# Kernel optimization log

Hardware: AMD Instinct MI355X
Metric: run time of the kernel (lower is better)

Reference implementation:

```python
import jax, jax.numpy as jnp
import numpy as np

N = 100000        # nodes
E = 1600000       # edges (avg degree 16)
H = 128           # gnn_hidden_size
F_NODE = 4        # node_features (forced to 4 by _validate_and_fix_data)
F_EDGE = 2        # edge_features (forced to 2)
L = 3             # gnn_layers
BN_EPS = 1e-5
NORM_EPS = 1e-12


def _sage_layer(h, src, dst, eattr, Wn, Ws, gamma, beta):
    # message: lin_neighbor(concat(x_j, edge_attr)) where x_j = h[src]
    msg = jnp.concatenate([h[src], eattr], axis=-1) @ Wn          # [E+N, H]
    agg = jax.ops.segment_sum(msg, dst, num_segments=N)           # scatter-sum
    cnt = jax.ops.segment_sum(jnp.ones(dst.shape[0], h.dtype), dst, num_segments=N)
    agg = agg / jnp.maximum(cnt, 1.0)[:, None]                    # mean aggregation
    out = jax.nn.relu(agg + h @ Ws)                               # self-loop linear + ReLU
    # BatchNorm1d (batch statistics, biased var)
    mean = out.mean(axis=0)
    var = out.var(axis=0)
    out = (out - mean) * jax.lax.rsqrt(var + BN_EPS) * gamma + beta
    # dropout = identity (eval); L2 normalize per node
    nrm = jnp.maximum(jnp.linalg.norm(out, axis=-1, keepdims=True), NORM_EPS)
    return out / nrm


def setup_inputs() -> dict:
    key = jax.random.key(0)
    ks = jax.random.split(key, 24)
    s = 0.05
    inp = {
        "x": jax.random.normal(ks[0], (N, F_NODE), jnp.float32),
        "edge_index": jax.random.randint(ks[1], (2, E), 0, N, dtype=jnp.int32),
        "edge_attr": jax.random.uniform(ks[2], (E, F_EDGE), jnp.float32),
        "W_in": jax.random.normal(ks[3], (F_NODE, H), jnp.float32) * s,
        "b_in": jnp.zeros((H,), jnp.float32),
        "W_jump": jax.random.normal(ks[4], (L * H, H), jnp.float32) * s,
        "b_jump": jnp.zeros((H,), jnp.float32),
        "W1": jax.random.normal(ks[5], (H, H // 2), jnp.float32) * s,
        "b1": jnp.zeros((H // 2,), jnp.float32),
        "W2": jax.random.normal(ks[6], (H // 2, 1), jnp.float32) * s,
        "b2": jnp.zeros((1,), jnp.float32),
    }
    for l in range(L):
        inp[f"Wn_{l}"] = jax.random.normal(ks[7 + 4 * l], (H + F_EDGE, H), jnp.float32) * s
        inp[f"Ws_{l}"] = jax.random.normal(ks[8 + 4 * l], (H, H), jnp.float32) * s
        inp[f"gamma_{l}"] = jnp.ones((H,), jnp.float32)
        inp[f"beta_{l}"] = jnp.zeros((H,), jnp.float32)
    return inp


def reference(x, edge_index, edge_attr, W_in, b_in,
              Wn_0, Ws_0, gamma_0, beta_0,
              Wn_1, Ws_1, gamma_1, beta_1,
              Wn_2, Ws_2, gamma_2, beta_2,
              W_jump, b_jump, W1, b1, W2, b2):
    # add self loops (with zero edge_attr), as in _safe_add_self_loops
    loop = jnp.arange(N, dtype=edge_index.dtype)
    src = jnp.concatenate([edge_index[0], loop])
    dst = jnp.concatenate([edge_index[1], loop])
    eattr = jnp.concatenate([edge_attr, jnp.zeros((N, F_EDGE), edge_attr.dtype)], axis=0)

    h = x @ W_in + b_in                                          # input_projection
    layer_params = [(Wn_0, Ws_0, gamma_0, beta_0),
                    (Wn_1, Ws_1, gamma_1, beta_1),
                    (Wn_2, Ws_2, gamma_2, beta_2)]
    layer_outputs = []
    for Wn, Ws, gamma, beta in layer_params:
        h = _sage_layer(h, src, dst, eattr, Wn, Ws, gamma, beta)
        layer_outputs.append(h)
    # jump (skip) connection: concat all layer outputs -> Linear -> ReLU
    h = jax.nn.relu(jnp.concatenate(layer_outputs, axis=-1) @ W_jump + b_jump)
    # neighbor_scorer: Linear -> ReLU -> Linear -> scalar per node
    scores = jax.nn.relu(h @ W1 + b1) @ W2 + b2                  # [N, 1]
    return scores[:, 0]
```

## Files before the change

### kernel.cpp

```cpp
#include <hip/hip_runtime.h>


#define HDIM 128

using f16x8 = __attribute__((ext_vector_type(8))) _Float16;
using f32x4 = __attribute__((ext_vector_type(4))) float;

__device__ inline unsigned pack_f16x2(float a, float b) {
  _Float16 ha = (_Float16)a, hb = (_Float16)b;
  unsigned short ua = __builtin_bit_cast(unsigned short, ha);
  unsigned short ub = __builtin_bit_cast(unsigned short, hb);
  return (unsigned)ua | ((unsigned)ub << 16);
}
__device__ inline float2 unpack_f16x2(unsigned u) {
  _Float16 lo = __builtin_bit_cast(_Float16, (unsigned short)(u & 0xffffu));
  _Float16 hi = __builtin_bit_cast(_Float16, (unsigned short)(u >> 16));
  return make_float2((float)lo, (float)hi);
}

__global__ __launch_bounds__(256) void count_kernel(
    const int* __restrict__ dst, int* __restrict__ cnt,
    int* __restrict__ rank, int E) {
  int e = blockIdx.x * 256 + threadIdx.x;
  if (e >= E) return;
  rank[e] = atomicAdd(&cnt[dst[e]], 1);
}

__global__ __launch_bounds__(128) void scan_block_sum(
    const int* __restrict__ cnt, int* __restrict__ bsum, int N) {
  __shared__ int sd[128];
  int t = threadIdx.x;
  int i = blockIdx.x * 128 + t;
  sd[t] = (i < N) ? cnt[i] : 0;
  __syncthreads();
  for (int off = 64; off > 0; off >>= 1) {
    if (t < off) sd[t] += sd[t + off];
    __syncthreads();
  }
  if (t == 0) bsum[blockIdx.x] = sd[0];
}

__global__ __launch_bounds__(256) void scan_partials(
    const int* __restrict__ bsum, int* __restrict__ boff, int nch) {
  __shared__ int sd[256];
  int t = threadIdx.x;
  int base = t * 4;
  int v0 = (base + 0 < nch) ? bsum[base + 0] : 0;
  int v1 = (base + 1 < nch) ? bsum[base + 1] : 0;
  int v2 = (base + 2 < nch) ? bsum[base + 2] : 0;
  int v3 = (base + 3 < nch) ? bsum[base + 3] : 0;
  sd[t] = v0 + v1 + v2 + v3;
  __syncthreads();
  for (int off = 1; off < 256; off <<= 1) {
    int x = sd[t];
    int y = (t >= off) ? sd[t - off] : 0;
    __syncthreads();
    sd[t] = x + y;
    __syncthreads();
  }
  int run = (t == 0) ? 0 : sd[t - 1];
  if (base + 0 < nch) boff[base + 0] = run; run += v0;
  if (base + 1 < nch) boff[base + 1] = run; run += v1;
  if (base + 2 < nch) boff[base + 2] = run; run += v2;
  if (base + 3 < nch) boff[base + 3] = run;
}

__global__ __launch_bounds__(128) void scan_final(
    const int* __restrict__ cnt, const int* __restrict__ boff,
    int* __restrict__ rs, int N) {
  __shared__ int sd[128];
  int t = threadIdx.x, b = blockIdx.x;
  int i = b * 128 + t;
  int v = (i < N) ? cnt[i] : 0;
  sd[t] = v;
  __syncthreads();
  for (int off = 1; off < 128; off <<= 1) {
    int x = sd[t];
    int y = (t >= off) ? sd[t - off] : 0;
    __syncthreads();
    sd[t] = x + y;
    __syncthreads();
  }
  if (i < N) rs[i] = boff[b] + ((t == 0) ? 0 : sd[t - 1]);
}

__global__ __launch_bounds__(256) void fill_kernel(
    const int* __restrict__ src, const int* __restrict__ dst,
    const float* __restrict__ ea, const int* __restrict__ rs,
    const int* __restrict__ rank, uint2* __restrict__ cidx2, int E) {
  int e = blockIdx.x * 256 + threadIdx.x;
  if (e >= E) return;
  int d = dst[e];
  float2 v = *reinterpret_cast<const float2*>(&ea[2 * (size_t)e]);
  int pos = rs[d] + rank[e];
  cidx2[pos] = make_uint2((unsigned)src[e], pack_f16x2(v.x, v.y));
}

__global__ __launch_bounds__(256) void aggx_kernel(
    const float* __restrict__ x, const int* __restrict__ rs,
    const int* __restrict__ cnt, const uint2* __restrict__ cidx2,
    float* __restrict__ aggx, float* __restrict__ eagg, int N) {
  int i = blockIdx.x * 256 + threadIdx.x;
  if (i >= N) return;
  float4 a = *reinterpret_cast<const float4*>(&x[(size_t)i * 4]);
  float4 b = make_float4(0.f, 0.f, 0.f, 0.f);
  float e0 = 0.f, e1 = 0.f, f0 = 0.f, f1 = 0.f;
  int p = rs[i], e = p + cnt[i];
  for (; p + 1 < e; p += 2) {
    uint2 c0 = cidx2[p], c1 = cidx2[p + 1];
    float4 v0 = *reinterpret_cast<const float4*>(&x[(size_t)c0.x * 4]);
    float4 v1 = *reinterpret_cast<const float4*>(&x[(size_t)c1.x * 4]);
    float2 u0 = unpack_f16x2(c0.y);
    float2 u1 = unpack_f16x2(c1.y);
    a.x += v0.x; a.y += v0.y; a.z += v0.z; a.w += v0.w;
    b.x += v1.x; b.y += v1.y; b.z += v1.z; b.w += v1.w;
    e0 += u0.x; e1 += u0.y;
    f0 += u1.x; f1 += u1.y;
  }
  if (p < e) {
    uint2 c0 = cidx2[p];
    float4 v0 = *reinterpret_cast<const float4*>(&x[(size_t)c0.x * 4]);
    float2 u0 = unpack_f16x2(c0.y);
    a.x += v0.x; a.y += v0.y; a.z += v0.z; a.w += v0.w;
    e0 += u0.x; e1 += u0.y;
  }
  a.x += b.x; a.y += b.y; a.z += b.z; a.w += b.w;
  *reinterpret_cast<float4*>(&aggx[(size_t)i * 4]) = a;
  eagg[2 * (size_t)i + 0] = e0 + f0;
  eagg[2 * (size_t)i + 1] = e1 + f1;
}

__global__ __launch_bounds__(256) void pack_weights_kernel(
    const float* __restrict__ Wn0, const float* __restrict__ Ws0,
    const float* __restrict__ Wn1, const float* __restrict__ Ws1,
    const float* __restrict__ Wn2, const float* __restrict__ Ws2,
    const float* __restrict__ Wj, _Float16* __restrict__ outp) {
  int i = blockIdx.x * 256 + threadIdx.x;
  if (i >= 147456) return;
  int j = i & 7, lane = (i >> 3) & 63;
  float v;
  if (i < 98304) {
    int l = i >> 15;
    int r = i & 32767;
    int nt = (r >> 9) & 7, kt = r >> 12;
    int k = kt * 32 + (lane >> 4) * 8 + j;
    int n = nt * 16 + (lane & 15);
    const float* Wn = (l == 0) ? Wn0 : (l == 1) ? Wn1 : Wn2;
    const float* Ws = (l == 0) ? Ws0 : (l == 1) ? Ws1 : Ws2;
    v = (k < 128) ? Wn[(size_t)k * HDIM + n] : Ws[(size_t)(k - 128) * HDIM + n];
  } else {
    int r = i - 98304;
    int nt = (r >> 9) & 7, kt = r >> 12;
    int k = kt * 32 + (lane >> 4) * 8 + j;
    int n = nt * 16 + (lane & 15);
    v = Wj[(size_t)k * HDIM + n];
  }
  outp[i] = (_Float16)v;
}

template <bool L0>
__global__ __launch_bounds__(256) void sage_mfma_kernel(
    const float* __restrict__ A0f, const float* __restrict__ A1f,
    const _Float16* __restrict__ Hprev, const int* __restrict__ rs,
    const uint2* __restrict__ cidx2,
    const float* __restrict__ Wi, const float* __restrict__ bi,
    const float* __restrict__ eagg, const int* __restrict__ cnt,
    const _Float16* __restrict__ Bp, const float* __restrict__ Wn,
    _Float16* __restrict__ outh, float* __restrict__ bnstat, int N) {
  __shared__ _Float16 sA[64 * 256];
  __shared__ float sE[128];
  __shared__ float sBNs[4][128];
  __shared__ float sBNq[4][128];
  const int t = threadIdx.x;
  const int base = blockIdx.x * 64;

  if (t < 64) {
    int grow = base + t;
    float e0 = 0.f, e1 = 0.f;
    if (grow < N) {
      float inv = 1.0f / ((float)cnt[grow] + 1.0f);
      e0 = eagg[2 * (size_t)grow] * inv;
      e1 = eagg[2 * (size_t)grow + 1] * inv;
    }
    sE[2 * t] = e0;
    sE[2 * t + 1] = e1;
  }

  if (L0) {
#pragma unroll
    for (int it = 0; it < 8; ++it) {
      int c = t + it * 256;
      int row = c >> 5, k8 = c & 31;
      int grow = base + row;
      f16x8 hv = {};
      if (grow < N) {
        float inv = 1.0f / ((float)cnt[grow] + 1.0f);
        float scale = (k8 < 16) ? inv : 1.0f;
        const float* rp = (k8 < 16) ? &A0f[(size_t)grow * 4] : &A1f[(size_t)grow * 4];
        float4 r = *reinterpret_cast<const float4*>(rp);
        int col0 = (k8 & 15) * 8;
#pragma unroll
        for (int jj = 0; jj < 8; ++jj) {
          int col = col0 + jj;
          hv[jj] = (_Float16)(bi[col] + scale * (r.x * Wi[col] + r.y * Wi[HDIM + col] +
                                                 r.z * Wi[2 * HDIM + col] + r.w * Wi[3 * HDIM + col]));
        }
      }
      int byte = (row * 512 + k8 * 16) ^ ((row & 7) << 4);
      *reinterpret_cast<f16x8*>(reinterpret_cast<char*>(sA) + byte) = hv;
    }
  } else {
    const int row = t >> 2, o = t & 3;
    const int grow = base + row;
    float acc[32];
#pragma unroll
    for (int c = 0; c < 32; ++c) acc[c] = 0.f;
    f16x8 selfv[4] = {};
    if (grow < N) {
      const char* selfrow = reinterpret_cast<const char*>(Hprev + (size_t)grow * HDIM);
#pragma unroll
      for (int j = 0; j < 4; ++j) {
        selfv[j] = *reinterpret_cast<const f16x8*>(selfrow + j * 64 + o * 16);
#pragma unroll
        for (int jj = 0; jj < 8; ++jj) acc[j * 8 + jj] = (float)selfv[j][jj];
      }
      int p = rs[grow];
      const int cn = cnt[grow];
      int e = p + cn;
      for (; p + 3 < e; p += 4) {
        uint2 q0 = cidx2[p], q1 = cidx2[p + 1], q2 = cidx2[p + 2], q3 = cidx2[p + 3];
        const char* m0 = reinterpret_cast<const char*>(Hprev + (size_t)q0.x * HDIM) + o * 16;
        const char* m1 = reinterpret_cast<const char*>(Hprev + (size_t)q1.x * HDIM) + o * 16;
        const char* m2 = reinterpret_cast<const char*>(Hprev + (size_t)q2.x * HDIM) + o * 16;
        const char* m3 = reinterpret_cast<const char*>(Hprev + (size_t)q3.x * HDIM) + o * 16;
        f16x8 c0[4], c1[4], c2[4], c3[4];
#pragma unroll
        for (int j = 0; j < 4; ++j) c0[j] = *reinterpret_cast<const f16x8*>(m0 + j * 64);
#pragma unroll
        for (int j = 0; j < 4; ++j) c1[j] = *reinterpret_cast<const f16x8*>(m1 + j * 64);
#pragma unroll
        for (int j = 0; j < 4; ++j) c2[j] = *reinterpret_cast<const f16x8*>(m2 + j * 64);
#pragma unroll
        for (int j = 0; j < 4; ++j) c3[j] = *reinterpret_cast<const f16x8*>(m3 + j * 64);
#pragma unroll
        for (int j = 0; j < 4; ++j)
#pragma unroll
          for (int jj = 0; jj < 8; ++jj)
            acc[j * 8 + jj] += ((float)c0[j][jj] + (float)c1[j][jj]) +
                               ((float)c2[j][jj] + (float)c3[j][jj]);
      }
      for (; p < e; ++p) {
        uint2 q0 = cidx2[p];
        const char* m0 = reinterpret_cast<const char*>(Hprev + (size_t)q0.x * HDIM) + o * 16;
#pragma unroll
        for (int j = 0; j < 4; ++j) {
          f16x8 c0 = *reinterpret_cast<const f16x8*>(m0 + j * 64);
#pragma unroll
          for (int jj = 0; jj < 8; ++jj) acc[j * 8 + jj] += (float)c0[jj];
        }
      }
      float inv = 1.0f / ((float)cn + 1.0f);
#pragma unroll
      for (int c = 0; c < 32; ++c) acc[c] *= inv;
    }
    const int swz = (row & 7) << 4;
#pragma unroll
    for (int j = 0; j < 4; ++j) {
      f16x8 av;
#pragma unroll
      for (int jj = 0; jj < 8; ++jj) av[jj] = (_Float16)acc[j * 8 + jj];
      int k8a = o + j * 4;
      *reinterpret_cast<f16x8*>(reinterpret_cast<char*>(sA) +
                                ((row * 512 + k8a * 16) ^ swz)) = av;
      int k8h = 16 + o + j * 4;
      *reinterpret_cast<f16x8*>(reinterpret_cast<char*>(sA) +
                                ((row * 512 + k8h * 16) ^ swz)) = selfv[j];
    }
  }
  __syncthreads();

  const int lane = t & 63;
  const int w = t >> 6;
  const int col16 = lane & 15;
  const int kgrp = lane >> 4;
  f32x4 acc[8];
#pragma unroll
  for (int nt = 0; nt < 8; ++nt) acc[nt] = (f32x4){0.f, 0.f, 0.f, 0.f};

  const int arow = w * 16 + col16;
  const int aswz = (arow & 7) << 4;
#pragma unroll
  for (int kt = 0; kt < 8; ++kt) {
    int abyte = (arow * 512 + kt * 64 + kgrp * 16) ^ aswz;
    f16x8 a = *reinterpret_cast<const f16x8*>(reinterpret_cast<const char*>(sA) + abyte);
    const f16x8* bp = reinterpret_cast<const f16x8*>(Bp) + (size_t)kt * 512 + lane;
#pragma unroll
    for (int nt = 0; nt < 8; ++nt) {
      f16x8 b = bp[nt * 64];
      acc[nt] = __builtin_amdgcn_mfma_f32_16x16x32_f16(a, b, acc[nt], 0, 0, 0);
    }
  }

#pragma unroll
  for (int nt = 0; nt < 8; ++nt) {
    int col = nt * 16 + col16;
    float we0 = Wn[(size_t)128 * HDIM + col];
    float we1 = Wn[(size_t)129 * HDIM + col];
    float s = 0.f, q = 0.f;
#pragma unroll
    for (int i = 0; i < 4; ++i) {
      int lr = w * 16 + kgrp * 4 + i;
      int row = base + lr;
      if (row < N) {
        float v = acc[nt][i] + sE[2 * lr] * we0 + sE[2 * lr + 1] * we1;
        v = fmaxf(v, 0.f);
        outh[(size_t)row * HDIM + col] = (_Float16)v;
        s += v;
        q += v * v;
      }
    }
    s += __shfl_xor(s, 16, 64);
    s += __shfl_xor(s, 32, 64);
    q += __shfl_xor(q, 16, 64);
    q += __shfl_xor(q, 32, 64);
    if (lane < 16) {
      sBNs[w][col] = s;
      sBNq[w][col] = q;
    }
  }
  __syncthreads();
  if (t < 128) {
    float s = sBNs[0][t] + sBNs[1][t] + sBNs[2][t] + sBNs[3][t];
    float q = sBNq[0][t] + sBNq[1][t] + sBNq[2][t] + sBNq[3][t];
    atomicAdd(&bnstat[t], s);
    atomicAdd(&bnstat[HDIM + t], q);
  }
}

__global__ __launch_bounds__(256) void bn_l2_kernel(
    const _Float16* __restrict__ outh, const float* __restrict__ stat,
    const float* __restrict__ gamma, const float* __restrict__ beta,
    float invN, _Float16* __restrict__ h, int N) {
  __shared__ float sAB[256];
  int t = threadIdx.x;
  if (t < 128) {
    float mean = stat[t] * invN;
    float var = stat[128 + t] * invN - mean * mean;
    float A = gamma[t] / sqrtf(var + 1e-5f);
    sAB[t] = A;
    sAB[128 + t] = beta[t] - mean * A;
  }
  __syncthreads();
  int i = blockIdx.x * 4 + (t >> 6);
  if (i >= N) return;
  int lane = t & 63;
  unsigned u = (reinterpret_cast<const unsigned*>(outh + (size_t)i * HDIM))[lane];
  float2 v = unpack_f16x2(u);
  float A0 = sAB[lane * 2 + 0], A1 = sAB[lane * 2 + 1];
  float B0 = sAB[128 + lane * 2 + 0], B1 = sAB[128 + lane * 2 + 1];
  float y0 = v.x * A0 + B0;
  float y1 = v.y * A1 + B1;
  float s = y0 * y0 + y1 * y1;
#pragma unroll
  for (int m = 32; m > 0; m >>= 1) s += __shfl_xor(s, m, 64);
  float inv = 1.0f / fmaxf(sqrtf(s), 1e-12f);
  (reinterpret_cast<unsigned*>(h + (size_t)i * HDIM))[lane] =
      pack_f16x2(y0 * inv, y1 * inv);
}

__global__ __launch_bounds__(256) void jump_mfma_kernel(
    const _Float16* __restrict__ h1, const _Float16* __restrict__ h2,
    const _Float16* __restrict__ h3, const _Float16* __restrict__ Bp,
    const float* __restrict__ bj, const float* __restrict__ W1p,
    const float* __restrict__ b1p, const float* __restrict__ W2p,
    const float* __restrict__ b2p, float* __restrict__ outp, int N) {
  __shared__ _Float16 sA[64 * 384];
  const int t = threadIdx.x;
  const int base = blockIdx.x * 64;

  const _Float16* hs[3] = {h1, h2, h3};
#pragma unroll
  for (int it = 0; it < 12; ++it) {
    int c = t + it * 256;
    int row = c / 48, k8 = c % 48;
    int grow = base + row;
    f16x8 hv = {};
    if (grow < N)
      hv = (reinterpret_cast<const f16x8*>(hs[k8 >> 4] + (size_t)grow * HDIM))[k8 & 15];
    int byte = (row * 768 + k8 * 16) ^ ((row & 7) << 4);
    *reinterpret_cast<f16x8*>(reinterpret_cast<char*>(sA) + byte) = hv;
  }
  __syncthreads();

  const int lane = t & 63;
  const int w = t >> 6;
  const int col16 = lane & 15;
  const int kgrp = lane >> 4;
  f32x4 acc[8];
#pragma unroll
  for (int nt = 0; nt < 8; ++nt) acc[nt] = (f32x4){0.f, 0.f, 0.f, 0.f};

  const int arow = w * 16 + col16;
  const int aswz = (arow & 7) << 4;
#pragma unroll
  for (int kt = 0; kt < 12; ++kt) {
    int abyte = (arow * 768 + kt * 64 + kgrp * 16) ^ aswz;
    f16x8 a = *reinterpret_cast<const f16x8*>(reinterpret_cast<const char*>(sA) + abyte);
    const f16x8* bp = reinterpret_cast<const f16x8*>(Bp) + (size_t)kt * 512 + lane;
#pragma unroll
    for (int nt = 0; nt < 8; ++nt) {
      f16x8 b = bp[nt * 64];
      acc[nt] = __builtin_amdgcn_mfma_f32_16x16x32_f16(a, b, acc[nt], 0, 0, 0);
    }
  }
  __syncthreads();

  float* sG = reinterpret_cast<float*>(sA);
  float* sS = sG + 64 * 128;
#pragma unroll
  for (int nt = 0; nt < 8; ++nt) {
    int col = nt * 16 + col16;
    float bb = bj[col];
#pragma unroll
    for (int i = 0; i < 4; ++i) {
      int lr = w * 16 + kgrp * 4 + i;
      sG[lr * 128 + col] = fmaxf(acc[nt][i] + bb, 0.f);
    }
  }
  __syncthreads();

  const int m = t & 63, grp = t >> 6;
  float a2[16];
#pragma unroll
  for (int i = 0; i < 16; ++i) a2[i] = b1p[m];
#pragma unroll 4
  for (int k = 0; k < 128; ++k) {
    float wv = W1p[(size_t)k * 64 + m];
#pragma unroll
    for (int i = 0; i < 16; ++i) a2[i] += sG[(grp * 16 + i) * 128 + k] * wv;
  }
#pragma unroll
  for (int i = 0; i < 16; ++i) sS[(grp * 16 + i) * 64 + m] = fmaxf(a2[i], 0.f);
  __syncthreads();

  if (t < 64) {
    int row = base + t;
    if (row < N) {
      float s = b2p[0];
#pragma unroll 8
      for (int mm = 0; mm < 64; ++mm) s += sS[t * 64 + mm] * W2p[mm];
      outp[row] = s;
    }
  }
}

extern "C" void kernel_launch(void* const* d_in, const int* in_sizes, int n_in,
                              void* d_out, int out_size, void* d_ws, size_t ws_size,
                              hipStream_t stream) {
  const float* x      = (const float*)d_in[0];
  const int*   ei     = (const int*)d_in[1];
  const float* eattr  = (const float*)d_in[2];
  const float* W_in   = (const float*)d_in[3];
  const float* b_in   = (const float*)d_in[4];
  const float* W_jump = (const float*)d_in[5];
  const float* b_jump = (const float*)d_in[6];
  const float* W1     = (const float*)d_in[7];
  const float* b1     = (const float*)d_in[8];
  const float* W2     = (const float*)d_in[9];
  const float* b2     = (const float*)d_in[10];
  const float* Wn[3] = {(const float*)d_in[11], (const float*)d_in[15], (const float*)d_in[19]};
  const float* Ws[3] = {(const float*)d_in[12], (const float*)d_in[16], (const float*)d_in[20]};
  const float* gm[3] = {(const float*)d_in[13], (const float*)d_in[17], (const float*)d_in[21]};
  const float* bt[3] = {(const float*)d_in[14], (const float*)d_in[18], (const float*)d_in[22]};

  const int N = in_sizes[0] / 4;
  const int E = in_sizes[2] / 2;
  const int* srcp = ei;
  const int* dstp = ei + (size_t)E;
  const int nch = (N + 127) / 128;
  const size_t nh = (size_t)N * HDIM;

  char* wsb = (char*)d_ws;
  size_t off = 0;
  auto carve = [&](size_t bytes) -> void* {
    void* p = wsb + off;
    off = (off + bytes + 255) & ~(size_t)255;
    return p;
  };
  _Float16* h1   = (_Float16*)carve(nh * 2);
  _Float16* h2   = (_Float16*)carve(nh * 2);
  _Float16* h3   = (_Float16*)carve(nh * 2);
  _Float16* outh = (_Float16*)carve(nh * 2);
  float*    aggx = (float*)carve((size_t)N * 4 * 4);
  float*    eagg = (float*)carve((size_t)N * 2 * 4);
  int*      cnt  = (int*)carve((size_t)N * 4);
  int*      rowstart = (int*)carve((size_t)N * 4);
  int*      rank     = (int*)carve((size_t)E * 4);
  uint2*    cidx2    = (uint2*)carve((size_t)E * 8);
  int*      bsum = (int*)carve(4096);
  int*      boff = (int*)carve(4096);
  float*    bnstat = (float*)carve(3 * 256 * sizeof(float));
  _Float16* wpack  = (_Float16*)carve(147456 * 2);

  hipMemsetAsync(cnt, 0, (size_t)N * sizeof(int), stream);
  hipMemsetAsync(bnstat, 0, 3 * 256 * sizeof(float), stream);
  count_kernel<<<(E + 255) / 256, 256, 0, stream>>>(dstp, cnt, rank, E);
  pack_weights_kernel<<<(147456 + 255) / 256, 256, 0, stream>>>(
      Wn[0], Ws[0], Wn[1], Ws[1], Wn[2], Ws[2], W_jump, wpack);
  scan_block_sum<<<nch, 128, 0, stream>>>(cnt, bsum, N);
  scan_partials<<<1, 256, 0, stream>>>(bsum, boff, nch);
  scan_final<<<nch, 128, 0, stream>>>(cnt, boff, rowstart, N);
  fill_kernel<<<(E + 255) / 256, 256, 0, stream>>>(srcp, dstp, eattr, rowstart, rank, cidx2, E);

  const int gemm_grid = (N + 63) / 64;
  const float invN = 1.0f / (float)N;

  aggx_kernel<<<(N + 255) / 256, 256, 0, stream>>>(x, rowstart, cnt, cidx2, aggx, eagg, N);
  sage_mfma_kernel<true><<<gemm_grid, 256, 0, stream>>>(
      aggx, x, nullptr, rowstart, cidx2, W_in, b_in, eagg, cnt, wpack, Wn[0],
      outh, bnstat, N);
  bn_l2_kernel<<<(N + 3) / 4, 256, 0, stream>>>(outh, bnstat, gm[0], bt[0], invN, h1, N);

  _Float16* hbuf[3] = {h1, h2, h3};
  for (int l = 1; l < 3; ++l) {
    sage_mfma_kernel<false><<<gemm_grid, 256, 0, stream>>>(
        nullptr, nullptr, hbuf[l - 1], rowstart, cidx2, nullptr, nullptr, eagg, cnt,
        wpack + (size_t)l * 32768, Wn[l], outh, bnstat + 256 * l, N);
    bn_l2_kernel<<<(N + 3) / 4, 256, 0, stream>>>(outh, bnstat + 256 * l,
                                                  gm[l], bt[l], invN, hbuf[l], N);
  }

  jump_mfma_kernel<<<gemm_grid, 256, 0, stream>>>(h1, h2, h3, wpack + 98304, b_jump,
                                                  W1, b1, W2, b2, (float*)d_out, N);
}
```

Before: 556.6 us.

## Shard degree-count atomics and process nodes in degree-sorted order

Count atomics are spread over 8 shard copies of the count array to cut contention, then summed, with per-shard offsets used in the CSR fill. A degree histogram and counting sort build a permutation so the aggregation kernels handle nodes of similar degree together, reducing wavefront divergence in the gather loops. The fill uses nontemporal stores. The trade-off is several extra small kernels, an 8x larger count buffer, and scattered output rows in the sage kernel.

```diff
diff --git a/kernel.cpp b/kernel.cpp
--- a/kernel.cpp
+++ b/kernel.cpp
@@ -2,6 +2,7 @@
 
 
 #define HDIM 128
+#define DEGB 512
 
 using f16x8 = __attribute__((ext_vector_type(8))) _Float16;
 using f32x4 = __attribute__((ext_vector_type(4))) float;
@@ -19,11 +20,32 @@
 }
 
 __global__ __launch_bounds__(256) void count_kernel(
-    const int* __restrict__ dst, int* __restrict__ cnt,
-    int* __restrict__ rank, int E) {
+    const int* __restrict__ dst, int* __restrict__ cnt8,
+    int* __restrict__ rank, int E, int N) {
   int e = blockIdx.x * 256 + threadIdx.x;
   if (e >= E) return;
-  rank[e] = atomicAdd(&cnt[dst[e]], 1);
+  int shard = blockIdx.x & 7;
+  rank[e] = atomicAdd(&cnt8[(size_t)shard * N + dst[e]], 1);
+}
+
+__global__ __launch_bounds__(256) void sum8_kernel(
+    int* __restrict__ cnt8, int* __restrict__ cnt, int N) {
+  int i = blockIdx.x * 256 + threadIdx.x;
+  if (i >= N) return;
+  int v[8];
+  int s = 0;
+#pragma unroll
+  for (int k = 0; k < 8; ++k) {
+    v[k] = cnt8[(size_t)k * N + i];
+    s += v[k];
+  }
+  cnt[i] = s;
+  int run = 0;
+#pragma unroll
+  for (int k = 0; k < 8; ++k) {
+    cnt8[(size_t)k * N + i] = run;
+    run += v[k];
+  }
 }
 
 __global__ __launch_bounds__(128) void scan_block_sum(
@@ -84,24 +106,79 @@
   if (i < N) rs[i] = boff[b] + ((t == 0) ? 0 : sd[t - 1]);
 }
 
+__global__ __launch_bounds__(256) void deg_hist_kernel(
+    const int* __restrict__ cnt, int* __restrict__ hist, int N) {
+  __shared__ int lh[DEGB];
+  int t = threadIdx.x;
+  for (int k = t; k < DEGB; k += 256) lh[k] = 0;
+  __syncthreads();
+  int i = blockIdx.x * 256 + t;
+  if (i < N) {
+    int d = cnt[i];
+    if (d > DEGB - 1) d = DEGB - 1;
+    atomicAdd(&lh[d], 1);
+  }
+  __syncthreads();
+  for (int k = t; k < DEGB; k += 256)
+    if (lh[k]) atomicAdd(&hist[k], lh[k]);
+}
+
+__global__ __launch_bounds__(256) void deg_scan_kernel(
+    const int* __restrict__ hist, int* __restrict__ degcur) {
+  __shared__ int sd[DEGB];
+  int t = threadIdx.x;
+  sd[t] = hist[t];
+  sd[t + 256] = hist[t + 256];
+  __syncthreads();
+  if (t == 0) {
+    int run = 0;
+    for (int k = 0; k < DEGB; ++k) {
+      int v = sd[k];
+      sd[k] = run;
+      run += v;
+    }
+  }
+  __syncthreads();
+  degcur[t] = sd[t];
+  degcur[t + 256] = sd[t + 256];
+}
+
+__global__ __launch_bounds__(256) void deg_scatter_kernel(
+    const int* __restrict__ cnt, int* __restrict__ degcur,
+    int* __restrict__ perm, int N) {
+  int i = blockIdx.x * 256 + threadIdx.x;
+  if (i >= N) return;
+  int d = cnt[i];
+  if (d > DEGB - 1) d = DEGB - 1;
+  int pos = atomicAdd(&degcur[d], 1);
+  perm[pos] = i;
+}
+
 __global__ __launch_bounds__(256) void fill_kernel(
     const int* __restrict__ src, const int* __restrict__ dst,
     const float* __restrict__ ea, const int* __restrict__ rs,
-    const int* __restrict__ rank, uint2* __restrict__ cidx2, int E) {
+    const int* __restrict__ cnt8, const int* __restrict__ rank,
+    unsigned long long* __restrict__ cidx2, int E, int N) {
   int e = blockIdx.x * 256 + threadIdx.x;
   if (e >= E) return;
+  int shard = blockIdx.x & 7;
   int d = dst[e];
   float2 v = *reinterpret_cast<const float2*>(&ea[2 * (size_t)e]);
-  int pos = rs[d] + rank[e];
-  cidx2[pos] = make_uint2((unsigned)src[e], pack_f16x2(v.x, v.y));
+  int pos = rs[d] + cnt8[(size_t)shard * N + d] + rank[e];
+  unsigned long long u =
+      (unsigned long long)(unsigned)src[e] |
+      ((unsigned long long)pack_f16x2(v.x, v.y) << 32);
+  __builtin_nontemporal_store(u, cidx2 + pos);
 }
 
 __global__ __launch_bounds__(256) void aggx_kernel(
     const float* __restrict__ x, const int* __restrict__ rs,
     const int* __restrict__ cnt, const uint2* __restrict__ cidx2,
+    const int* __restrict__ perm,
     float* __restrict__ aggx, float* __restrict__ eagg, int N) {
-  int i = blockIdx.x * 256 + threadIdx.x;
-  if (i >= N) return;
+  int idx = blockIdx.x * 256 + threadIdx.x;
+  if (idx >= N) return;
+  int i = perm[idx];
   float4 a = *reinterpret_cast<const float4*>(&x[(size_t)i * 4]);
   float4 b = make_float4(0.f, 0.f, 0.f, 0.f);
   float e0 = 0.f, e1 = 0.f, f0 = 0.f, f1 = 0.f;
@@ -162,7 +239,7 @@
 __global__ __launch_bounds__(256) void sage_mfma_kernel(
     const float* __restrict__ A0f, const float* __restrict__ A1f,
     const _Float16* __restrict__ Hprev, const int* __restrict__ rs,
-    const uint2* __restrict__ cidx2,
+    const uint2* __restrict__ cidx2, const int* __restrict__ perm,
     const float* __restrict__ Wi, const float* __restrict__ bi,
     const float* __restrict__ eagg, const int* __restrict__ cnt,
     const _Float16* __restrict__ Bp, const float* __restrict__ Wn,
@@ -175,9 +252,10 @@
   const int base = blockIdx.x * 64;
 
   if (t < 64) {
-    int grow = base + t;
+    int gidx = base + t;
     float e0 = 0.f, e1 = 0.f;
-    if (grow < N) {
+    if (gidx < N) {
+      int grow = L0 ? gidx : perm[gidx];
       float inv = 1.0f / ((float)cnt[grow] + 1.0f);
       e0 = eagg[2 * (size_t)grow] * inv;
       e1 = eagg[2 * (size_t)grow + 1] * inv;
@@ -211,12 +289,13 @@
     }
   } else {
     const int row = t >> 2, o = t & 3;
-    const int grow = base + row;
+    const int gidx = base + row;
     float acc[32];
 #pragma unroll
     for (int c = 0; c < 32; ++c) acc[c] = 0.f;
     f16x8 selfv[4] = {};
-    if (grow < N) {
+    if (gidx < N) {
+      const int grow = perm[gidx];
       const char* selfrow = reinterpret_cast<const char*>(Hprev + (size_t)grow * HDIM);
 #pragma unroll
       for (int j = 0; j < 4; ++j) {
@@ -310,8 +389,9 @@
 #pragma unroll
     for (int i = 0; i < 4; ++i) {
       int lr = w * 16 + kgrp * 4 + i;
-      int row = base + lr;
-      if (row < N) {
+      int gidx = base + lr;
+      if (gidx < N) {
+        int row = L0 ? gidx : perm[gidx];
         float v = acc[nt][i] + sE[2 * lr] * we0 + sE[2 * lr + 1] * we1;
         v = fmaxf(v, 0.f);
         outh[(size_t)row * HDIM + col] = (_Float16)v;
@@ -494,38 +574,50 @@
   float*    aggx = (float*)carve((size_t)N * 4 * 4);
   float*    eagg = (float*)carve((size_t)N * 2 * 4);
   int*      cnt  = (int*)carve((size_t)N * 4);
+  int*      cnt8 = (int*)carve((size_t)N * 8 * 4);
   int*      rowstart = (int*)carve((size_t)N * 4);
+  int*      perm     = (int*)carve((size_t)N * 4);
   int*      rank     = (int*)carve((size_t)E * 4);
-  uint2*    cidx2    = (uint2*)carve((size_t)E * 8);
+  unsigned long long* cidx2 = (unsigned long long*)carve((size_t)E * 8);
   int*      bsum = (int*)carve(4096);
   int*      boff = (int*)carve(4096);
+  int*      hist = (int*)carve(DEGB * 4);
+  int*      degcur = (int*)carve(DEGB * 4);
   float*    bnstat = (float*)carve(3 * 256 * sizeof(float));
   _Float16* wpack  = (_Float16*)carve(147456 * 2);
 
-  hipMemsetAsync(cnt, 0, (size_t)N * sizeof(int), stream);
+  hipMemsetAsync(cnt8, 0, (size_t)N * 8 * sizeof(int), stream);
+  hipMemsetAsync(hist, 0, DEGB * sizeof(int), stream);
   hipMemsetAsync(bnstat, 0, 3 * 256 * sizeof(float), stream);
-  count_kernel<<<(E + 255) / 256, 256, 0, stream>>>(dstp, cnt, rank, E);
+  count_kernel<<<(E + 255) / 256, 256, 0, stream>>>(dstp, cnt8, rank, E, N);
   pack_weights_kernel<<<(147456 + 255) / 256, 256, 0, stream>>>(
       Wn[0], Ws[0], Wn[1], Ws[1], Wn[2], Ws[2], W_jump, wpack);
+  sum8_kernel<<<(N + 255) / 256, 256, 0, stream>>>(cnt8, cnt, N);
   scan_block_sum<<<nch, 128, 0, stream>>>(cnt, bsum, N);
   scan_partials<<<1, 256, 0, stream>>>(bsum, boff, nch);
   scan_final<<<nch, 128, 0, stream>>>(cnt, boff, rowstart, N);
-  fill_kernel<<<(E + 255) / 256, 256, 0, stream>>>(srcp, dstp, eattr, rowstart, rank, cidx2, E);
+  deg_hist_kernel<<<(N + 255) / 256, 256, 0, stream>>>(cnt, hist, N);
+  deg_scan_kernel<<<1, 256, 0, stream>>>(hist, degcur);
+  deg_scatter_kernel<<<(N + 255) / 256, 256, 0, stream>>>(cnt, degcur, perm, N);
+  fill_kernel<<<(E + 255) / 256, 256, 0, stream>>>(srcp, dstp, eattr, rowstart,
+                                                   cnt8, rank, cidx2, E, N);
 
   const int gemm_grid = (N + 63) / 64;
   const float invN = 1.0f / (float)N;
 
-  aggx_kernel<<<(N + 255) / 256, 256, 0, stream>>>(x, rowstart, cnt, cidx2, aggx, eagg, N);
+  aggx_kernel<<<(N + 255) / 256, 256, 0, stream>>>(x, rowstart, cnt,
+                                                   (const uint2*)cidx2, perm, aggx, eagg, N);
   sage_mfma_kernel<true><<<gemm_grid, 256, 0, stream>>>(
-      aggx, x, nullptr, rowstart, cidx2, W_in, b_in, eagg, cnt, wpack, Wn[0],
-      outh, bnstat, N);
+      aggx, x, nullptr, rowstart, (const uint2*)cidx2, nullptr, W_in, b_in,
+      eagg, cnt, wpack, Wn[0], outh, bnstat, N);
   bn_l2_kernel<<<(N + 3) / 4, 256, 0, stream>>>(outh, bnstat, gm[0], bt[0], invN, h1, N);
 
   _Float16* hbuf[3] = {h1, h2, h3};
   for (int l = 1; l < 3; ++l) {
     sage_mfma_kernel<false><<<gemm_grid, 256, 0, stream>>>(
-        nullptr, nullptr, hbuf[l - 1], rowstart, cidx2, nullptr, nullptr, eagg, cnt,
-        wpack + (size_t)l * 32768, Wn[l], outh, bnstat + 256 * l, N);
+        nullptr, nullptr, hbuf[l - 1], rowstart, (const uint2*)cidx2, perm,
+        nullptr, nullptr, eagg, cnt, wpack + (size_t)l * 32768, Wn[l],
+        outh, bnstat + 256 * l, N);
     bn_l2_kernel<<<(N + 3) / 4, 256, 0, stream>>>(outh, bnstat + 256 * l,
                                                   gm[l], bt[l], invN, hbuf[l], N);
   }
```

New measurement: 866.8 us. +55.7%, slower.
